# Kernel optimization log

Hardware: AMD Instinct MI355X
Metric: run time of the kernel (lower is better)

## Reference

```python
import jax, jax.numpy as jnp
import numpy as np
import math

H = 16
EPS = 1e-5

def _layernorm(x, g, b):
    mu = jnp.mean(x, axis=-1, keepdims=True)
    var = jnp.var(x, axis=-1, keepdims=True)
    return (x - mu) * jax.lax.rsqrt(var + EPS) * g + b

def setup_inputs() -> dict:
    key = jax.random.key(0)
    ks = jax.random.split(key, 8)
    B, S, D, F, M = 2, 2048, 1024, 4096, 64
    dh = D // H
    s = 1.0 / math.sqrt(D)
    return {
        "x": jax.random.normal(ks[0], (B, S, D), jnp.float32),
        "Wq": jax.random.normal(ks[1], (D, D), jnp.float32) * s,
        "Wk": jax.random.normal(ks[2], (D, D), jnp.float32) * s,
        "Wv": jax.random.normal(ks[3], (D, D), jnp.float32) * s,
        "Wo": jax.random.normal(ks[4], (D, D), jnp.float32) * s,
        "Mk": jax.random.normal(ks[5], (H, dh, M), jnp.float32) / math.sqrt(dh),
        "ln1_g": jnp.ones((D,), jnp.float32),
        "ln1_b": jnp.zeros((D,), jnp.float32),
        "ln2_g": jnp.ones((D,), jnp.float32),
        "ln2_b": jnp.zeros((D,), jnp.float32),
        "W1": jax.random.normal(ks[6], (D, F), jnp.float32) * s,
        "b1": jnp.zeros((F,), jnp.float32),
        "W2": jax.random.normal(ks[7], (F, D), jnp.float32) / math.sqrt(F),
        "b2": jnp.zeros((D,), jnp.float32),
    }

def reference(x, Wq, Wk, Wv, Wo, Mk, ln1_g, ln1_b, ln2_g, ln2_b, W1, b1, W2, b2):
    B, S, D = x.shape
    dh = D // H
    def split(t):  # (B,S,D) -> (B,H,S,dh)
        return t.reshape(B, S, H, dh).transpose(0, 2, 1, 3)
    qh = split(x @ Wq)
    kh = split(x @ Wk)
    vh = split(x @ Wv)
    q_mem = jnp.einsum('bhsd,hdm->bhsm', qh, Mk)
    k_mem = jnp.einsum('bhsd,hdm->bhsm', kh, Mk)
    attn = jnp.einsum('bhsm,bhtm->bhst', q_mem, k_mem) / math.sqrt(dh)
    attn = jax.nn.softmax(attn, axis=-1)
    ctx = jnp.einsum('bhst,bhtd->bhsd', attn, vh)
    ctx = ctx.transpose(0, 2, 1, 3).reshape(B, S, D)
    x = _layernorm(x + ctx @ Wo, ln1_g, ln1_b)
    ff = jax.nn.gelu(x @ W1 + b1, approximate=False) @ W2 + b2
    return _layernorm(x + ff, ln2_g, ln2_b)
```

## Files before the change

### kernel.cpp

```cpp
#include <hip/hip_runtime.h>
#include <math.h>

#define NH 16
#define DH 64
#define MDIM 64
#define DMODEL 1024
#define FDIM 4096
#define BATCH 2
#define SEQ 2048
#define NROWS (BATCH*SEQ)

typedef short bf16x8 __attribute__((ext_vector_type(8)));
typedef float f32x4 __attribute__((ext_vector_type(4)));

__device__ __forceinline__ float gelu_f(float v) {
    return 0.5f * v * (1.0f + erff(v * 0.70710678118654752f));
}
__device__ __forceinline__ ushort f2bf(float f) {
    union { float f; unsigned u; } v; v.f = f;
    unsigned r = v.u + 0x7fffu + ((v.u >> 16) & 1u);
    return (ushort)(r >> 16);
}
__device__ __forceinline__ float bf2f(ushort h) {
    union { unsigned u; float f; } v; v.u = ((unsigned)h) << 16;
    return v.f;
}
__device__ __forceinline__ void gl_lds16(const ushort* g, ushort* l) {
    __builtin_amdgcn_global_load_lds((const __attribute__((address_space(1))) void*)g,
                                     (__attribute__((address_space(3))) void*)l, 16, 0, 0);
}

__global__ __launch_bounds__(256)
void splitA_kernel(const float* __restrict__ X, ushort* __restrict__ hi,
                   ushort* __restrict__ lo, int n4) {
    int i = blockIdx.x * 256 + threadIdx.x;
    if (i >= n4) return;
    float4 v = ((const float4*)X)[i];
    ushort4 h, l;
    h.x = f2bf(v.x); l.x = f2bf(v.x - bf2f(h.x));
    h.y = f2bf(v.y); l.y = f2bf(v.y - bf2f(h.y));
    h.z = f2bf(v.z); l.z = f2bf(v.z - bf2f(h.z));
    h.w = f2bf(v.w); l.w = f2bf(v.w - bf2f(h.w));
    ((ushort4*)hi)[i] = h;
    ((ushort4*)lo)[i] = l;
}

__global__ __launch_bounds__(256)
void splitT_kernel(const float* __restrict__ W, ushort* __restrict__ Thi,
                   ushort* __restrict__ Tlo, int K, int N) {
    __shared__ float tile[64][65];
    const int n0 = blockIdx.x * 64;
    const int k0 = blockIdx.y * 64;
    const int t  = threadIdx.x;
    const int r  = t >> 4;
    const int c4 = (t & 15) * 4;
#pragma unroll
    for (int i = 0; i < 4; ++i) {
        int row = r + i * 16;
        float4 v = *(const float4*)&W[(size_t)(k0 + row) * N + n0 + c4];
        tile[c4 + 0][row] = v.x;
        tile[c4 + 1][row] = v.y;
        tile[c4 + 2][row] = v.z;
        tile[c4 + 3][row] = v.w;
    }
    __syncthreads();
#pragma unroll
    for (int i = 0; i < 4; ++i) {
        int row = r + i * 16;
        float a = tile[row][c4 + 0], b = tile[row][c4 + 1];
        float c = tile[row][c4 + 2], d = tile[row][c4 + 3];
        ushort4 h, l;
        h.x = f2bf(a); l.x = f2bf(a - bf2f(h.x));
        h.y = f2bf(b); l.y = f2bf(b - bf2f(h.y));
        h.z = f2bf(c); l.z = f2bf(c - bf2f(h.z));
        h.w = f2bf(d); l.w = f2bf(d - bf2f(h.w));
        size_t off = (size_t)(n0 + row) * K + k0 + c4;
        *(ushort4*)&Thi[off] = h;
        *(ushort4*)&Tlo[off] = l;
    }
}

template<int ACT, int SPLIT_OUT>
__global__ __launch_bounds__(256)
void mfma_gemm(const ushort* __restrict__ Ahi, const ushort* __restrict__ Alo,
               const ushort* __restrict__ BThi, const ushort* __restrict__ BTlo,
               const float* __restrict__ bias, float* __restrict__ C,
               ushort* __restrict__ Chi, ushort* __restrict__ Clo,
               int K, int N) {
    __shared__ ushort As[128 * 32];
    __shared__ ushort Bs[128 * 32];
    const int t    = threadIdx.x;
    const int lane = t & 63;
    const int wid  = t >> 6;
    const int wr   = wid >> 1;
    const int wc   = wid & 1;
    const int i0   = blockIdx.y * 128;
    const int n0   = blockIdx.x * 128;
    const int srow = t >> 2;
    const int scol = (t & 3) * 8;
    ushort* aDst0 = As + t * 8;
    ushort* aDst1 = As + 2048 + t * 8;
    ushort* bDst0 = Bs + t * 8;
    ushort* bDst1 = Bs + 2048 + t * 8;

    f32x4 acc[4][4];
#pragma unroll
    for (int m = 0; m < 4; ++m)
#pragma unroll
        for (int n = 0; n < 4; ++n) {
            acc[m][n][0] = 0.f; acc[m][n][1] = 0.f;
            acc[m][n][2] = 0.f; acc[m][n][3] = 0.f;
        }

    const int aOff = (wr * 64 + (lane & 15)) * 32 + (lane >> 4) * 8;
    const int bOff = (wc * 64 + (lane & 15)) * 32 + (lane >> 4) * 8;

    for (int seg = 0; seg < 3; ++seg) {
        const ushort* Ab = (seg == 1) ? Alo : Ahi;
        const ushort* Bb = (seg == 2) ? BTlo : BThi;
        const ushort* Ap0 = Ab + (size_t)(i0 + srow) * K + scol;
        const ushort* Ap1 = Ap0 + (size_t)64 * K;
        const ushort* Bp0 = Bb + (size_t)(n0 + srow) * K + scol;
        const ushort* Bp1 = Bp0 + (size_t)64 * K;
        for (int k0 = 0; k0 < K; k0 += 32) {
            __syncthreads();
            gl_lds16(Ap0 + k0, aDst0);
            gl_lds16(Ap1 + k0, aDst1);
            gl_lds16(Bp0 + k0, bDst0);
            gl_lds16(Bp1 + k0, bDst1);
            __syncthreads();
            bf16x8 af[4], bfr[4];
#pragma unroll
            for (int m = 0; m < 4; ++m)
                af[m] = *(const bf16x8*)&As[aOff + m * 16 * 32];
#pragma unroll
            for (int n = 0; n < 4; ++n)
                bfr[n] = *(const bf16x8*)&Bs[bOff + n * 16 * 32];
#pragma unroll
            for (int m = 0; m < 4; ++m)
#pragma unroll
                for (int n = 0; n < 4; ++n)
                    acc[m][n] = __builtin_amdgcn_mfma_f32_16x16x32_bf16(af[m], bfr[n], acc[m][n], 0, 0, 0);
        }
    }

    const int orow  = i0 + wr * 64 + (lane >> 4) * 4;
    const int ocol0 = n0 + wc * 64 + (lane & 15);
#pragma unroll
    for (int n = 0; n < 4; ++n) {
        const int colg = ocol0 + n * 16;
        float bv = bias ? bias[colg] : 0.f;
#pragma unroll
        for (int m = 0; m < 4; ++m) {
#pragma unroll
            for (int r = 0; r < 4; ++r) {
                const int rowg = orow + m * 16 + r;
                float v = acc[m][n][r] + bv;
                if (ACT == 1) v = gelu_f(v);
                size_t off = (size_t)rowg * N + colg;
                if (SPLIT_OUT) {
                    ushort h = f2bf(v);
                    Chi[off] = h;
                    Clo[off] = f2bf(v - bf2f(h));
                } else {
                    C[off] = v;
                }
            }
        }
    }
}

__global__ __launch_bounds__(256)
void headproj_kernel(const float* __restrict__ X, int xstride, const float* __restrict__ Mk,
                     ushort* __restrict__ oh, ushort* __restrict__ ol) {
    __shared__ float Qs[64][65];
    __shared__ float Ms[64][68];
    const int s0 = blockIdx.x * 64;
    const int h  = blockIdx.y;
    const int b  = blockIdx.z;
    const int t  = threadIdx.x;
    const int tc = t & 15, tr = t >> 4;
    const float* xb = X + (size_t)(b * SEQ + s0) * xstride + h * 64;
    const float* mk = Mk + (size_t)h * 64 * 64;
#pragma unroll
    for (int i = 0; i < 4; ++i) {
        int e4  = t + i * 256;
        int row = e4 >> 4;
        int c4  = (e4 & 15) << 2;
        float4 q4 = *(const float4*)(xb + (size_t)row * xstride + c4);
        Qs[c4 + 0][row] = q4.x;
        Qs[c4 + 1][row] = q4.y;
        Qs[c4 + 2][row] = q4.z;
        Qs[c4 + 3][row] = q4.w;
        float4 m4 = *(const float4*)(mk + row * 64 + c4);
        *(float4*)&Ms[row][c4] = m4;
    }
    __syncthreads();
    float acc[4][4] = {};
#pragma unroll 16
    for (int kk = 0; kk < 64; ++kk) {
        float a0 = Qs[kk][tr * 4 + 0];
        float a1 = Qs[kk][tr * 4 + 1];
        float a2 = Qs[kk][tr * 4 + 2];
        float a3 = Qs[kk][tr * 4 + 3];
        float4 b4 = *(const float4*)&Ms[kk][tc * 4];
        acc[0][0] += a0 * b4.x; acc[0][1] += a0 * b4.y; acc[0][2] += a0 * b4.z; acc[0][3] += a0 * b4.w;
        acc[1][0] += a1 * b4.x; acc[1][1] += a1 * b4.y; acc[1][2] += a1 * b4.z; acc[1][3] += a1 * b4.w;
        acc[2][0] += a2 * b4.x; acc[2][1] += a2 * b4.y; acc[2][2] += a2 * b4.z; acc[2][3] += a2 * b4.w;
        acc[3][0] += a3 * b4.x; acc[3][1] += a3 * b4.y; acc[3][2] += a3 * b4.z; acc[3][3] += a3 * b4.w;
    }
    ushort* oph = oh + ((size_t)(b * NH + h) * SEQ + s0) * 64;
    ushort* opl = ol + ((size_t)(b * NH + h) * SEQ + s0) * 64;
#pragma unroll
    for (int i = 0; i < 4; ++i) {
        ushort4 h4, l4;
        h4.x = f2bf(acc[i][0]); l4.x = f2bf(acc[i][0] - bf2f(h4.x));
        h4.y = f2bf(acc[i][1]); l4.y = f2bf(acc[i][1] - bf2f(h4.y));
        h4.z = f2bf(acc[i][2]); l4.z = f2bf(acc[i][2] - bf2f(h4.z));
        h4.w = f2bf(acc[i][3]); l4.w = f2bf(acc[i][3] - bf2f(h4.w));
        *(ushort4*)(oph + (size_t)(tr * 4 + i) * 64 + tc * 4) = h4;
        *(ushort4*)(opl + (size_t)(tr * 4 + i) * 64 + tc * 4) = l4;
    }
}

__global__ __launch_bounds__(256)
void vsplitT_kernel(const float* __restrict__ qkv, ushort* __restrict__ vth,
                    ushort* __restrict__ vtl) {
    __shared__ float tile[64][65];
    const int s0 = blockIdx.x * 64;
    const int h  = blockIdx.y;
    const int b  = blockIdx.z;
    const int t  = threadIdx.x;
    const int r  = t >> 4;
    const int c4 = (t & 15) * 4;
    const float* src = qkv + (size_t)(b * SEQ + s0) * 3072 + 2048 + h * 64;
#pragma unroll
    for (int i = 0; i < 4; ++i) {
        int srow = r + i * 16;
        float4 v = *(const float4*)(src + (size_t)srow * 3072 + c4);
        tile[c4 + 0][srow] = v.x;
        tile[c4 + 1][srow] = v.y;
        tile[c4 + 2][srow] = v.z;
        tile[c4 + 3][srow] = v.w;
    }
    __syncthreads();
    const size_t obase = (size_t)(b * NH + h) * 64 * SEQ + s0;
#pragma unroll
    for (int i = 0; i < 4; ++i) {
        int d = r + i * 16;
        float a = tile[d][c4 + 0], bb = tile[d][c4 + 1];
        float c = tile[d][c4 + 2], dd = tile[d][c4 + 3];
        ushort4 h4, l4;
        h4.x = f2bf(a);  l4.x = f2bf(a - bf2f(h4.x));
        h4.y = f2bf(bb); l4.y = f2bf(bb - bf2f(h4.y));
        h4.z = f2bf(c);  l4.z = f2bf(c - bf2f(h4.z));
        h4.w = f2bf(dd); l4.w = f2bf(dd - bf2f(h4.w));
        *(ushort4*)&vth[obase + (size_t)d * SEQ + c4] = h4;
        *(ushort4*)&vtl[obase + (size_t)d * SEQ + c4] = l4;
    }
}

__global__ __launch_bounds__(64)
void attn_mfma(const ushort* __restrict__ qmh, const ushort* __restrict__ qml,
               const ushort* __restrict__ kmh, const ushort* __restrict__ kml,
               const ushort* __restrict__ vth, const ushort* __restrict__ vtl,
               ushort* __restrict__ ctx_hi, ushort* __restrict__ ctx_lo) {
    __shared__ ushort ph[1024];
    __shared__ ushort pl[1024];
    const int q0 = blockIdx.x * 16;
    const int h  = blockIdx.y;
    const int b  = blockIdx.z;
    const int lane = threadIdx.x;
    const int rg = lane >> 4;
    const int lc = lane & 15;
    const size_t bh = (size_t)b * NH + h;

    const ushort* qb_h = qmh + (bh * SEQ + q0 + lc) * 64 + rg * 8;
    const ushort* qb_l = qml + (bh * SEQ + q0 + lc) * 64 + rg * 8;
    bf16x8 qfh[2], qfl[2];
    qfh[0] = *(const bf16x8*)(qb_h);
    qfh[1] = *(const bf16x8*)(qb_h + 32);
    qfl[0] = *(const bf16x8*)(qb_l);
    qfl[1] = *(const bf16x8*)(qb_l + 32);

    const ushort* kb_h = kmh + (bh * SEQ + lc) * 64 + rg * 8;
    const ushort* kb_l = kml + (bh * SEQ + lc) * 64 + rg * 8;
    const ushort* vb_h = vth + (bh * 64 + lc) * SEQ + rg * 8;
    const ushort* vb_l = vtl + (bh * 64 + lc) * SEQ + rg * 8;

    f32x4 ctx[4];
#pragma unroll
    for (int n = 0; n < 4; ++n) { ctx[n][0] = 0.f; ctx[n][1] = 0.f; ctx[n][2] = 0.f; ctx[n][3] = 0.f; }
    float m_r[4] = { -INFINITY, -INFINITY, -INFINITY, -INFINITY };
    float l_r[4] = { 0.f, 0.f, 0.f, 0.f };

    bf16x8 kh[4][2], kl[4][2];
#pragma unroll
    for (int n = 0; n < 4; ++n) {
        kh[n][0] = *(const bf16x8*)(kb_h + (size_t)(16 * n) * 64);
        kh[n][1] = *(const bf16x8*)(kb_h + (size_t)(16 * n) * 64 + 32);
        kl[n][0] = *(const bf16x8*)(kb_l + (size_t)(16 * n) * 64);
        kl[n][1] = *(const bf16x8*)(kb_l + (size_t)(16 * n) * 64 + 32);
    }

    for (int kv0 = 0; kv0 < SEQ; kv0 += 64) {
        bf16x8 vh[4][2];
#pragma unroll
        for (int n = 0; n < 4; ++n) {
            vh[n][0] = *(const bf16x8*)(vb_h + (size_t)(16 * n) * SEQ + kv0);
            vh[n][1] = *(const bf16x8*)(vb_h + (size_t)(16 * n) * SEQ + kv0 + 32);
        }
        f32x4 sacc[4];
#pragma unroll
        for (int n = 0; n < 4; ++n) { sacc[n][0] = 0.f; sacc[n][1] = 0.f; sacc[n][2] = 0.f; sacc[n][3] = 0.f; }
#pragma unroll
        for (int n = 0; n < 4; ++n) {
            sacc[n] = __builtin_amdgcn_mfma_f32_16x16x32_bf16(qfh[0], kh[n][0], sacc[n], 0, 0, 0);
            sacc[n] = __builtin_amdgcn_mfma_f32_16x16x32_bf16(qfh[1], kh[n][1], sacc[n], 0, 0, 0);
            sacc[n] = __builtin_amdgcn_mfma_f32_16x16x32_bf16(qfl[0], kh[n][0], sacc[n], 0, 0, 0);
            sacc[n] = __builtin_amdgcn_mfma_f32_16x16x32_bf16(qfl[1], kh[n][1], sacc[n], 0, 0, 0);
            sacc[n] = __builtin_amdgcn_mfma_f32_16x16x32_bf16(qfh[0], kl[n][0], sacc[n], 0, 0, 0);
            sacc[n] = __builtin_amdgcn_mfma_f32_16x16x32_bf16(qfh[1], kl[n][1], sacc[n], 0, 0, 0);
        }
        if (kv0 + 64 < SEQ) {
            const size_t nb = (size_t)(kv0 + 64) * 64;
#pragma unroll
            for (int n = 0; n < 4; ++n) {
                kh[n][0] = *(const bf16x8*)(kb_h + nb + (size_t)(16 * n) * 64);
                kh[n][1] = *(const bf16x8*)(kb_h + nb + (size_t)(16 * n) * 64 + 32);
                kl[n][0] = *(const bf16x8*)(kb_l + nb + (size_t)(16 * n) * 64);
                kl[n][1] = *(const bf16x8*)(kb_l + nb + (size_t)(16 * n) * 64 + 32);
            }
        }
#pragma unroll
        for (int r = 0; r < 4; ++r) {
            float s0 = sacc[0][r] * 0.125f;
            float s1 = sacc[1][r] * 0.125f;
            float s2 = sacc[2][r] * 0.125f;
            float s3 = sacc[3][r] * 0.125f;
            float pm = fmaxf(fmaxf(s0, s1), fmaxf(s2, s3));
            pm = fmaxf(pm, __shfl_xor(pm, 1));
            pm = fmaxf(pm, __shfl_xor(pm, 2));
            pm = fmaxf(pm, __shfl_xor(pm, 4));
            pm = fmaxf(pm, __shfl_xor(pm, 8));
            float mnew  = fmaxf(m_r[r], pm);
            float alpha = __expf(m_r[r] - mnew);
            m_r[r] = mnew;
            float p0 = __expf(s0 - mnew);
            float p1 = __expf(s1 - mnew);
            float p2 = __expf(s2 - mnew);
            float p3 = __expf(s3 - mnew);
            float rs = p0 + p1 + p2 + p3;
            rs += __shfl_xor(rs, 1);
            rs += __shfl_xor(rs, 2);
            rs += __shfl_xor(rs, 4);
            rs += __shfl_xor(rs, 8);
            l_r[r] = l_r[r] * alpha + rs;
            ctx[0][r] *= alpha; ctx[1][r] *= alpha; ctx[2][r] *= alpha; ctx[3][r] *= alpha;
            const int q = rg * 4 + r;
            const int swz = (q & 7) << 3;
            const int rowb = q * 64;
            ushort hh;
            hh = f2bf(p0); ph[(rowb + lc)      ^ swz] = hh; pl[(rowb + lc)      ^ swz] = f2bf(p0 - bf2f(hh));
            hh = f2bf(p1); ph[(rowb + lc + 16) ^ swz] = hh; pl[(rowb + lc + 16) ^ swz] = f2bf(p1 - bf2f(hh));
            hh = f2bf(p2); ph[(rowb + lc + 32) ^ swz] = hh; pl[(rowb + lc + 32) ^ swz] = f2bf(p2 - bf2f(hh));
            hh = f2bf(p3); ph[(rowb + lc + 48) ^ swz] = hh; pl[(rowb + lc + 48) ^ swz] = f2bf(p3 - bf2f(hh));
        }
        bf16x8 vl[4][2];
#pragma unroll
        for (int n = 0; n < 4; ++n) {
            vl[n][0] = *(const bf16x8*)(vb_l + (size_t)(16 * n) * SEQ + kv0);
            vl[n][1] = *(const bf16x8*)(vb_l + (size_t)(16 * n) * SEQ + kv0 + 32);
        }
        bf16x8 pah[2], pal[2];
        {
            const int swz = (lc & 7) << 3;
            pah[0] = *(const bf16x8*)&ph[(lc * 64 + rg * 8)      ^ swz];
            pah[1] = *(const bf16x8*)&ph[(lc * 64 + rg * 8 + 32) ^ swz];
            pal[0] = *(const bf16x8*)&pl[(lc * 64 + rg * 8)      ^ swz];
            pal[1] = *(const bf16x8*)&pl[(lc * 64 + rg * 8 + 32) ^ swz];
        }
#pragma unroll
        for (int n = 0; n < 4; ++n) {
            ctx[n] = __builtin_amdgcn_mfma_f32_16x16x32_bf16(pah[0], vh[n][0], ctx[n], 0, 0, 0);
            ctx[n] = __builtin_amdgcn_mfma_f32_16x16x32_bf16(pah[1], vh[n][1], ctx[n], 0, 0, 0);
            ctx[n] = __builtin_amdgcn_mfma_f32_16x16x32_bf16(pal[0], vh[n][0], ctx[n], 0, 0, 0);
            ctx[n] = __builtin_amdgcn_mfma_f32_16x16x32_bf16(pal[1], vh[n][1], ctx[n], 0, 0, 0);
        }
#pragma unroll
        for (int n = 0; n < 4; ++n) {
            ctx[n] = __builtin_amdgcn_mfma_f32_16x16x32_bf16(pah[0], vl[n][0], ctx[n], 0, 0, 0);
            ctx[n] = __builtin_amdgcn_mfma_f32_16x16x32_bf16(pah[1], vl[n][1], ctx[n], 0, 0, 0);
        }
    }
#pragma unroll
    for (int r = 0; r < 4; ++r) {
        float inv = 1.0f / l_r[r];
        const int q = q0 + rg * 4 + r;
        size_t base = ((size_t)b * SEQ + q) * DMODEL + h * 64 + lc;
#pragma unroll
        for (int n = 0; n < 4; ++n) {
            float o = ctx[n][r] * inv;
            ushort hh = f2bf(o);
            ctx_hi[base + 16 * n] = hh;
            ctx_lo[base + 16 * n] = f2bf(o - bf2f(hh));
        }
    }
}

__global__ __launch_bounds__(256)
void ln_kernel(const float* __restrict__ X, const float* __restrict__ R,
               const float* __restrict__ gw, const float* __restrict__ bw,
               float* __restrict__ out, ushort* __restrict__ ohi, ushort* __restrict__ olo) {
    __shared__ float red[8];
    const int i = blockIdx.x;
    const int t = threadIdx.x;
    const float* xp = X + (size_t)i * DMODEL;
    const float* rp = R + (size_t)i * DMODEL;
    float4 xv = *(const float4*)(xp + t * 4);
    float4 rv = *(const float4*)(rp + t * 4);
    float v0 = xv.x + rv.x, v1 = xv.y + rv.y, v2 = xv.z + rv.z, v3 = xv.w + rv.w;
    float sum = v0 + v1 + v2 + v3;
    float sq  = v0 * v0 + v1 * v1 + v2 * v2 + v3 * v3;
#pragma unroll
    for (int off = 32; off > 0; off >>= 1) {
        sum += __shfl_down(sum, off, 64);
        sq  += __shfl_down(sq,  off, 64);
    }
    int wid = t >> 6;
    if ((t & 63) == 0) { red[wid] = sum; red[4 + wid] = sq; }
    __syncthreads();
    sum = red[0] + red[1] + red[2] + red[3];
    sq  = red[4] + red[5] + red[6] + red[7];
    float mu   = sum * (1.0f / DMODEL);
    float var  = sq * (1.0f / DMODEL) - mu * mu;
    float rstd = rsqrtf(var + 1e-5f);
    float4 gv = *(const float4*)(gw + t * 4);
    float4 bv = *(const float4*)(bw + t * 4);
    float4 o;
    o.x = (v0 - mu) * rstd * gv.x + bv.x;
    o.y = (v1 - mu) * rstd * gv.y + bv.y;
    o.z = (v2 - mu) * rstd * gv.z + bv.z;
    o.w = (v3 - mu) * rstd * gv.w + bv.w;
    *(float4*)(out + (size_t)i * DMODEL + t * 4) = o;
    if (ohi) {
        ushort4 h, l;
        h.x = f2bf(o.x); l.x = f2bf(o.x - bf2f(h.x));
        h.y = f2bf(o.y); l.y = f2bf(o.y - bf2f(h.y));
        h.z = f2bf(o.z); l.z = f2bf(o.z - bf2f(h.z));
        h.w = f2bf(o.w); l.w = f2bf(o.w - bf2f(h.w));
        size_t off = (size_t)i * DMODEL + t * 4;
        *(ushort4*)&ohi[off] = h;
        *(ushort4*)&olo[off] = l;
    }
}

extern "C" void kernel_launch(void* const* d_in, const int* in_sizes, int n_in,
                              void* d_out, int out_size, void* d_ws, size_t ws_size,
                              hipStream_t stream) {
    const float* x   = (const float*)d_in[0];
    const float* Wq  = (const float*)d_in[1];
    const float* Wk  = (const float*)d_in[2];
    const float* Wv  = (const float*)d_in[3];
    const float* Wo  = (const float*)d_in[4];
    const float* Mk  = (const float*)d_in[5];
    const float* g1  = (const float*)d_in[6];
    const float* bl1 = (const float*)d_in[7];
    const float* g2  = (const float*)d_in[8];
    const float* bl2 = (const float*)d_in[9];
    const float* W1  = (const float*)d_in[10];
    const float* bf1 = (const float*)d_in[11];
    const float* W2  = (const float*)d_in[12];
    const float* bf2 = (const float*)d_in[13];
    float* out = (float*)d_out;
    char* wsb  = (char*)d_ws;

    const size_t MB = 1024 * 1024;
    float*  qkv   = (float*)(wsb + 0 * MB);
    ushort* qmh   = (ushort*)(wsb + 48 * MB);
    ushort* qml   = (ushort*)(wsb + 56 * MB);
    ushort* kmh   = (ushort*)(wsb + 64 * MB);
    ushort* kml   = (ushort*)(wsb + 72 * MB);
    ushort* vth   = (ushort*)(wsb + 80 * MB);
    ushort* vtl   = (ushort*)(wsb + 88 * MB);
    ushort* x_hi  = (ushort*)(wsb + 96 * MB);
    ushort* x_lo  = (ushort*)(wsb + 104 * MB);
    ushort* ctx_hi = x_hi;
    ushort* ctx_lo = x_lo;
    float*  wo_out = (float*)(wsb + 112 * MB);
    float*  ff2    = wo_out;
    float*  y      = (float*)(wsb + 128 * MB);
    ushort* y_hi   = (ushort*)(wsb + 144 * MB);
    ushort* y_lo   = (ushort*)(wsb + 152 * MB);
    ushort* wqkvT_hi = (ushort*)(wsb + 160 * MB);
    ushort* wqkvT_lo = (ushort*)(wsb + 166 * MB);
    ushort* woT_hi   = (ushort*)(wsb + 172 * MB);
    ushort* woT_lo   = (ushort*)(wsb + 174 * MB);
    ushort* w1T_hi   = (ushort*)(wsb + 176 * MB);
    ushort* w1T_lo   = (ushort*)(wsb + 184 * MB);
    ushort* w2T_hi   = (ushort*)(wsb + 64 * MB);
    ushort* w2T_lo   = (ushort*)(wsb + 72 * MB);
    ushort* h1_hi    = (ushort*)(wsb + 0 * MB);
    ushort* h1_lo    = (ushort*)(wsb + 32 * MB);

    dim3 blk(256);
    dim3 hgrid(SEQ / 64, NH, BATCH);
    splitT_kernel<<<dim3(16, 16), blk, 0, stream>>>(Wq, wqkvT_hi, wqkvT_lo, DMODEL, DMODEL);
    splitT_kernel<<<dim3(16, 16), blk, 0, stream>>>(Wk, wqkvT_hi + (size_t)1024 * 1024, wqkvT_lo + (size_t)1024 * 1024, DMODEL, DMODEL);
    splitT_kernel<<<dim3(16, 16), blk, 0, stream>>>(Wv, wqkvT_hi + (size_t)2048 * 1024, wqkvT_lo + (size_t)2048 * 1024, DMODEL, DMODEL);
    splitT_kernel<<<dim3(16, 16), blk, 0, stream>>>(Wo, woT_hi, woT_lo, DMODEL, DMODEL);
    splitT_kernel<<<dim3(64, 16), blk, 0, stream>>>(W1, w1T_hi, w1T_lo, DMODEL, FDIM);
    splitA_kernel<<<dim3(4096), blk, 0, stream>>>(x, x_hi, x_lo, NROWS * DMODEL / 4);
    mfma_gemm<0, 0><<<dim3(24, 32), blk, 0, stream>>>(x_hi, x_lo, wqkvT_hi, wqkvT_lo,
                                                      nullptr, qkv, nullptr, nullptr, DMODEL, 3072);
    headproj_kernel<<<hgrid, blk, 0, stream>>>(qkv + 0,    3072, Mk, qmh, qml);
    headproj_kernel<<<hgrid, blk, 0, stream>>>(qkv + 1024, 3072, Mk, kmh, kml);
    vsplitT_kernel<<<hgrid, blk, 0, stream>>>(qkv, vth, vtl);
    attn_mfma<<<dim3(SEQ / 16, NH, BATCH), dim3(64), 0, stream>>>(qmh, qml, kmh, kml, vth, vtl, ctx_hi, ctx_lo);
    splitT_kernel<<<dim3(16, 64), blk, 0, stream>>>(W2, w2T_hi, w2T_lo, FDIM, DMODEL);
    mfma_gemm<0, 0><<<dim3(8, 32), blk, 0, stream>>>(ctx_hi, ctx_lo, woT_hi, woT_lo,
                                                     nullptr, wo_out, nullptr, nullptr, DMODEL, DMODEL);
    ln_kernel<<<dim3(NROWS), blk, 0, stream>>>(x, wo_out, g1, bl1, y, y_hi, y_lo);
    mfma_gemm<1, 1><<<dim3(32, 32), blk, 0, stream>>>(y_hi, y_lo, w1T_hi, w1T_lo,
                                                      bf1, nullptr, h1_hi, h1_lo, DMODEL, FDIM);
    mfma_gemm<0, 0><<<dim3(8, 32), blk, 0, stream>>>(h1_hi, h1_lo, w2T_hi, w2T_lo,
                                                     bf2, ff2, nullptr, nullptr, FDIM, DMODEL);
    ln_kernel<<<dim3(NROWS), blk, 0, stream>>>(y, ff2, g2, bl2, out, nullptr, nullptr);
}
```

Before: 1.201 ms.

## Fuse split-bf16 GEMM passes into one K loop and drop P low part

The GEMM kernel used to sweep K three times, once for each hi/lo product pair. It now loads the hi and lo tiles of A and B together in a single K loop and issues all three MFMAs per tile. This cuts the number of barriers and loop iterations, at the cost of more LDS and registers per block. The attention kernel also stops splitting the softmax probabilities into hi and lo bf16 parts, which removes the low-part LDS buffer and its MFMAs but lowers the accuracy of P·V.

```diff
diff --git a/kernel.cpp b/kernel.cpp
--- a/kernel.cpp
+++ b/kernel.cpp
@@ -87,8 +87,10 @@
                const float* __restrict__ bias, float* __restrict__ C,
                ushort* __restrict__ Chi, ushort* __restrict__ Clo,
                int K, int N) {
-    __shared__ ushort As[128 * 32];
-    __shared__ ushort Bs[128 * 32];
+    __shared__ ushort Ah[128 * 32];
+    __shared__ ushort Al[128 * 32];
+    __shared__ ushort Bh[128 * 32];
+    __shared__ ushort Bl[128 * 32];
     const int t    = threadIdx.x;
     const int lane = t & 63;
     const int wid  = t >> 6;
@@ -98,10 +100,20 @@
     const int n0   = blockIdx.x * 128;
     const int srow = t >> 2;
     const int scol = (t & 3) * 8;
-    ushort* aDst0 = As + t * 8;
-    ushort* aDst1 = As + 2048 + t * 8;
-    ushort* bDst0 = Bs + t * 8;
-    ushort* bDst1 = Bs + 2048 + t * 8;
+
+    ushort* dAh0 = Ah + t * 8;  ushort* dAh1 = Ah + 2048 + t * 8;
+    ushort* dAl0 = Al + t * 8;  ushort* dAl1 = Al + 2048 + t * 8;
+    ushort* dBh0 = Bh + t * 8;  ushort* dBh1 = Bh + 2048 + t * 8;
+    ushort* dBl0 = Bl + t * 8;  ushort* dBl1 = Bl + 2048 + t * 8;
+
+    const ushort* Aph0 = Ahi + (size_t)(i0 + srow) * K + scol;
+    const ushort* Aph1 = Aph0 + (size_t)64 * K;
+    const ushort* Apl0 = Alo + (size_t)(i0 + srow) * K + scol;
+    const ushort* Apl1 = Apl0 + (size_t)64 * K;
+    const ushort* Bph0 = BThi + (size_t)(n0 + srow) * K + scol;
+    const ushort* Bph1 = Bph0 + (size_t)64 * K;
+    const ushort* Bpl0 = BTlo + (size_t)(n0 + srow) * K + scol;
+    const ushort* Bpl1 = Bpl0 + (size_t)64 * K;
 
     f32x4 acc[4][4];
 #pragma unroll
@@ -115,33 +127,36 @@
     const int aOff = (wr * 64 + (lane & 15)) * 32 + (lane >> 4) * 8;
     const int bOff = (wc * 64 + (lane & 15)) * 32 + (lane >> 4) * 8;
 
-    for (int seg = 0; seg < 3; ++seg) {
-        const ushort* Ab = (seg == 1) ? Alo : Ahi;
-        const ushort* Bb = (seg == 2) ? BTlo : BThi;
-        const ushort* Ap0 = Ab + (size_t)(i0 + srow) * K + scol;
-        const ushort* Ap1 = Ap0 + (size_t)64 * K;
-        const ushort* Bp0 = Bb + (size_t)(n0 + srow) * K + scol;
-        const ushort* Bp1 = Bp0 + (size_t)64 * K;
-        for (int k0 = 0; k0 < K; k0 += 32) {
-            __syncthreads();
-            gl_lds16(Ap0 + k0, aDst0);
-            gl_lds16(Ap1 + k0, aDst1);
-            gl_lds16(Bp0 + k0, bDst0);
-            gl_lds16(Bp1 + k0, bDst1);
-            __syncthreads();
-            bf16x8 af[4], bfr[4];
-#pragma unroll
-            for (int m = 0; m < 4; ++m)
-                af[m] = *(const bf16x8*)&As[aOff + m * 16 * 32];
-#pragma unroll
-            for (int n = 0; n < 4; ++n)
-                bfr[n] = *(const bf16x8*)&Bs[bOff + n * 16 * 32];
-#pragma unroll
-            for (int m = 0; m < 4; ++m)
-#pragma unroll
-                for (int n = 0; n < 4; ++n)
-                    acc[m][n] = __builtin_amdgcn_mfma_f32_16x16x32_bf16(af[m], bfr[n], acc[m][n], 0, 0, 0);
-        }
+    for (int k0 = 0; k0 < K; k0 += 32) {
+        __syncthreads();
+        gl_lds16(Aph0 + k0, dAh0);
+        gl_lds16(Aph1 + k0, dAh1);
+        gl_lds16(Apl0 + k0, dAl0);
+        gl_lds16(Apl1 + k0, dAl1);
+        gl_lds16(Bph0 + k0, dBh0);
+        gl_lds16(Bph1 + k0, dBh1);
+        gl_lds16(Bpl0 + k0, dBl0);
+        gl_lds16(Bpl1 + k0, dBl1);
+        __syncthreads();
+        bf16x8 afh[4], afl[4], bfh[4], bfl[4];
+#pragma unroll
+        for (int m = 0; m < 4; ++m) {
+            afh[m] = *(const bf16x8*)&Ah[aOff + m * 16 * 32];
+            afl[m] = *(const bf16x8*)&Al[aOff + m * 16 * 32];
+        }
+#pragma unroll
+        for (int n = 0; n < 4; ++n) {
+            bfh[n] = *(const bf16x8*)&Bh[bOff + n * 16 * 32];
+            bfl[n] = *(const bf16x8*)&Bl[bOff + n * 16 * 32];
+        }
+#pragma unroll
+        for (int m = 0; m < 4; ++m)
+#pragma unroll
+            for (int n = 0; n < 4; ++n) {
+                acc[m][n] = __builtin_amdgcn_mfma_f32_16x16x32_bf16(afh[m], bfh[n], acc[m][n], 0, 0, 0);
+                acc[m][n] = __builtin_amdgcn_mfma_f32_16x16x32_bf16(afl[m], bfh[n], acc[m][n], 0, 0, 0);
+                acc[m][n] = __builtin_amdgcn_mfma_f32_16x16x32_bf16(afh[m], bfl[n], acc[m][n], 0, 0, 0);
+            }
     }
 
     const int orow  = i0 + wr * 64 + (lane >> 4) * 4;
@@ -266,7 +281,6 @@
                const ushort* __restrict__ vth, const ushort* __restrict__ vtl,
                ushort* __restrict__ ctx_hi, ushort* __restrict__ ctx_lo) {
     __shared__ ushort ph[1024];
-    __shared__ ushort pl[1024];
     const int q0 = blockIdx.x * 16;
     const int h  = blockIdx.y;
     const int b  = blockIdx.z;
@@ -360,11 +374,10 @@
             const int q = rg * 4 + r;
             const int swz = (q & 7) << 3;
             const int rowb = q * 64;
-            ushort hh;
-            hh = f2bf(p0); ph[(rowb + lc)      ^ swz] = hh; pl[(rowb + lc)      ^ swz] = f2bf(p0 - bf2f(hh));
-            hh = f2bf(p1); ph[(rowb + lc + 16) ^ swz] = hh; pl[(rowb + lc + 16) ^ swz] = f2bf(p1 - bf2f(hh));
-            hh = f2bf(p2); ph[(rowb + lc + 32) ^ swz] = hh; pl[(rowb + lc + 32) ^ swz] = f2bf(p2 - bf2f(hh));
-            hh = f2bf(p3); ph[(rowb + lc + 48) ^ swz] = hh; pl[(rowb + lc + 48) ^ swz] = f2bf(p3 - bf2f(hh));
+            ph[(rowb + lc)      ^ swz] = f2bf(p0);
+            ph[(rowb + lc + 16) ^ swz] = f2bf(p1);
+            ph[(rowb + lc + 32) ^ swz] = f2bf(p2);
+            ph[(rowb + lc + 48) ^ swz] = f2bf(p3);
         }
         bf16x8 vl[4][2];
 #pragma unroll
@@ -372,20 +385,16 @@
             vl[n][0] = *(const bf16x8*)(vb_l + (size_t)(16 * n) * SEQ + kv0);
             vl[n][1] = *(const bf16x8*)(vb_l + (size_t)(16 * n) * SEQ + kv0 + 32);
         }
-        bf16x8 pah[2], pal[2];
+        bf16x8 pah[2];
         {
             const int swz = (lc & 7) << 3;
             pah[0] = *(const bf16x8*)&ph[(lc * 64 + rg * 8)      ^ swz];
             pah[1] = *(const bf16x8*)&ph[(lc * 64 + rg * 8 + 32) ^ swz];
-            pal[0] = *(const bf16x8*)&pl[(lc * 64 + rg * 8)      ^ swz];
-            pal[1] = *(const bf16x8*)&pl[(lc * 64 + rg * 8 + 32) ^ swz];
         }
 #pragma unroll
         for (int n = 0; n < 4; ++n) {
             ctx[n] = __builtin_amdgcn_mfma_f32_16x16x32_bf16(pah[0], vh[n][0], ctx[n], 0, 0, 0);
             ctx[n] = __builtin_amdgcn_mfma_f32_16x16x32_bf16(pah[1], vh[n][1], ctx[n], 0, 0, 0);
-            ctx[n] = __builtin_amdgcn_mfma_f32_16x16x32_bf16(pal[0], vh[n][0], ctx[n], 0, 0, 0);
-            ctx[n] = __builtin_amdgcn_mfma_f32_16x16x32_bf16(pal[1], vh[n][1], ctx[n], 0, 0, 0);
         }
 #pragma unroll
         for (int n = 0; n < 4; ++n) {
```

Result: faster. 1.085 ms (-9.6%).
